# Kernel optimization log

Hardware: AMD Instinct MI355X
Metric: run time of the kernel (lower is better)

The kernel has to match this reference:

```python
import jax, jax.numpy as jnp
import numpy as np

B = 8192
D = 1024
NUM_CLASSES = 100


def setup_inputs() -> dict:
    key = jax.random.key(0)
    kx, ky = jax.random.split(key)
    x = jax.random.normal(kx, (B, D), dtype=jnp.float32)
    y = jax.random.randint(ky, (B,), 0, NUM_CLASSES, dtype=jnp.int64)
    return {"x": x, "y": y, "T": 1}


def reference(x, y, T):
    b = x.shape[0]
    # Pairwise Euclidean distances via Gram matrix (same math as
    # torch.norm(x[:,None]-x, dim=2) without the b*b*d intermediate).
    xn = jnp.sum(x * x, axis=1)                      # [b]
    d2 = xn[None, :] + xn[:, None] - 2.0 * (x @ x.T)  # [b, b]
    d2 = jnp.maximum(d2, 0.0)
    eye = jnp.eye(b, dtype=bool)
    # Diagonal is masked to -inf below; plug 1.0 to keep sqrt well-defined.
    dist = jnp.sqrt(jnp.where(eye, 1.0, d2))
    e_dist = -dist * T
    neg_inf = jnp.float32(-jnp.inf)
    # Denominator: all pairs except self.
    den_dist = jnp.where(eye, neg_inf, e_dist)
    # Numerator: same-label pairs except self.
    same = (y[None, :] == y[:, None]) & ~eye
    num_dist = jnp.where(same, e_dist, neg_inf)
    num = jax.nn.logsumexp(num_dist, axis=1)         # [b]
    den = jax.nn.logsumexp(den_dist, axis=1)         # [b]
    # Original fixup: anchors with no positives (num == -inf) contribute 0 to num;
    # den is re-indexed by isinf(num) AFTER num was zeroed, so den is unchanged.
    num = jnp.where(jnp.isinf(num), 0.0, num)
    return -jnp.mean(num - den)
```

## Files before the change

### kernel.cpp

```cpp
#include <hip/hip_runtime.h>
#include <hip/hip_bf16.h>
#include <stdint.h>

#define BN 8192
#define DK 1024
#define NTILES 2080

typedef __attribute__((ext_vector_type(4))) float f32x4;
typedef __attribute__((ext_vector_type(2))) long long2v;

__device__ __forceinline__ unsigned int f2e4m3(float f) {
  const unsigned int u = __float_as_uint(f);
  const unsigned int sign = (u >> 24) & 0x80u;
  float a = fabsf(f);
  if (a >= 448.f) return sign | 0x7Eu;
  if (a < 0.015625f) {
    int m = (int)rintf(a * 512.f);
    return sign | (unsigned int)m;
  }
  unsigned int x = __float_as_uint(a);
  x += 0x7FFFFu + ((x >> 20) & 1u);
  const unsigned int e = (x >> 23) - 127u + 7u;
  const unsigned int m = (x >> 20) & 7u;
  return sign | (e << 4) | m;
}

__global__ __launch_bounds__(256) void snn_prep(const float* __restrict__ x,
                                                unsigned char* __restrict__ xb,
                                                float* __restrict__ xn,
                                                float* __restrict__ den,
                                                float* __restrict__ num,
                                                float* __restrict__ out) {
  const int row = blockIdx.x * 4 + (threadIdx.x >> 6);
  const int lane = threadIdx.x & 63;
  const float4* src = (const float4*)(x + (size_t)row * DK) + lane * 4;
  float s = 0.f;
  unsigned int pk[4];
#pragma unroll
  for (int i = 0; i < 4; ++i) {
    float4 v = src[i];
    s = fmaf(v.x, v.x, s); s = fmaf(v.y, v.y, s);
    s = fmaf(v.z, v.z, s); s = fmaf(v.w, v.w, s);
    pk[i] = f2e4m3(v.x) | (f2e4m3(v.y) << 8) | (f2e4m3(v.z) << 16) |
            (f2e4m3(v.w) << 24);
  }
  const int g = lane >> 2;
  const int c = lane & 3;
  uint4 o; o.x = pk[0]; o.y = pk[1]; o.z = pk[2]; o.w = pk[3];
  *(uint4*)(xb + (size_t)row * DK + g * 64 + ((c ^ (row & 3)) << 4)) = o;
#pragma unroll
  for (int m = 32; m >= 1; m >>= 1) s += __shfl_xor(s, m);
  if (lane == 0) {
    xn[row] = s;
    den[row] = 0.f;
    num[row] = 0.f;
    if (row == 0) out[0] = 0.f;
  }
}

__global__ __launch_bounds__(256, 4) void snn_main(
    const unsigned char* __restrict__ xb, const float* __restrict__ xn,
    const int* __restrict__ y, const unsigned int* __restrict__ Tp,
    float* __restrict__ den, float* __restrict__ num) {
  __shared__ __align__(16) unsigned char As[2][128 * 64];
  __shared__ __align__(16) unsigned char Bs[2][128 * 64];
  __shared__ float xnA[128], xnB[128];
  __shared__ int yA[128], yB[128];

  const int t = threadIdx.x;
  const int lane = t & 63;
  const int w = t >> 6;
  const int wr = w >> 1, wc = w & 1;
  const int l15 = lane & 15;
  const int lg = lane >> 4;

  const int bid = blockIdx.x;
  const int ts = (bid & 7) * (NTILES / 8) + (bid >> 3);
  int I = (int)(64.5f - sqrtf(64.5f * 64.5f - 2.0f * (float)ts));
  while (I > 0 && (64 * I - (I * (I - 1)) / 2) > ts) --I;
  while ((64 * (I + 1) - ((I + 1) * I) / 2) <= ts) ++I;
  const int J = I + (ts - (64 * I - (I * (I - 1)) / 2));
  const int r0 = I * 128, c0 = J * 128;
  const bool diag = (I == J);

  const unsigned int tu = *Tp;
  const float tf = (tu & 0x7f800000u) ? __uint_as_float(tu) : (float)(int)tu;

  if (t < 128) {
    xnA[t] = xn[r0 + t]; yA[t] = y[r0 + t];
    xnB[t] = xn[c0 + t]; yB[t] = y[c0 + t];
  }

  auto ISSUE = [&](int buf, int kt) {
#pragma unroll
    for (int i = 0; i < 2; ++i) {
      const int linear = i * 256 + t;
      const int row = linear >> 2;
      const int cg = linear & 3;
      const unsigned char* sa = xb + (size_t)(r0 + row) * DK + kt + cg * 16;
      const unsigned char* sb = xb + (size_t)(c0 + row) * DK + kt + cg * 16;
      __builtin_amdgcn_global_load_lds(
          (const __attribute__((address_space(1))) void*)sa,
          (__attribute__((address_space(3))) void*)(As[buf] + linear * 16), 16, 0, 0);
      __builtin_amdgcn_global_load_lds(
          (const __attribute__((address_space(1))) void*)sb,
          (__attribute__((address_space(3))) void*)(Bs[buf] + linear * 16), 16, 0, 0);
    }
  };

  f32x4 acc[4][4];
#pragma unroll
  for (int mi = 0; mi < 4; ++mi)
#pragma unroll
    for (int ni = 0; ni < 4; ++ni) acc[mi][ni] = (f32x4){0.f, 0.f, 0.f, 0.f};

  const int fro = (lg ^ (l15 & 3)) << 4;

  ISSUE(0, 0);
  __syncthreads();

  for (int T = 0; T < 16; ++T) {
    const int buf = T & 1;
    if (T < 15) ISSUE(buf ^ 1, (T + 1) * 64);
    long2v aF[4], bF[4];
#pragma unroll
    for (int mi = 0; mi < 4; ++mi) {
      const int row = wr * 64 + mi * 16 + l15;
      aF[mi] = *(const long2v*)(As[buf] + row * 64 + fro);
    }
#pragma unroll
    for (int ni = 0; ni < 4; ++ni) {
      const int row = wc * 64 + ni * 16 + l15;
      bF[ni] = *(const long2v*)(Bs[buf] + row * 64 + fro);
    }
#pragma unroll
    for (int kk = 0; kk < 2; ++kk)
#pragma unroll
      for (int mi = 0; mi < 4; ++mi)
#pragma unroll
        for (int ni = 0; ni < 4; ++ni)
          acc[mi][ni] = __builtin_amdgcn_mfma_f32_16x16x32_fp8_fp8(
              aF[mi][kk], bF[ni][kk], acc[mi][ni], 0, 0, 0);
    __syncthreads();
  }

  float cxn[4]; int cy[4];
#pragma unroll
  for (int ni = 0; ni < 4; ++ni) {
    const int c_l = wc * 64 + ni * 16 + l15;
    cxn[ni] = xnB[c_l]; cy[ni] = yB[c_l];
  }
#pragma unroll
  for (int mi = 0; mi < 4; ++mi) {
#pragma unroll
    for (int rg = 0; rg < 4; ++rg) {
      const int row_l = wr * 64 + mi * 16 + lg * 4 + rg;
      const int rG = r0 + row_l;
      const float rxn = xnA[row_l];
      const int ry = yA[row_l];
      float u = 0.f, av = 0.f;
#pragma unroll
      for (int ni = 0; ni < 4; ++ni) {
        const int cG = c0 + wc * 64 + ni * 16 + l15;
        const float a = acc[mi][ni][rg];
        const float d2 = fmaxf(rxn + cxn[ni] - 2.0f * a, 0.f);
        const float p = (rG == cG) ? 0.f : __expf(-sqrtf(d2) * tf);
        const float v = (ry == cy[ni]) ? -p : p;
        acc[mi][ni][rg] = v;
        u += v; av += fabsf(v);
      }
#pragma unroll
      for (int mm = 8; mm >= 1; mm >>= 1) {
        u += __shfl_xor(u, mm); av += __shfl_xor(av, mm);
      }
      if (l15 == 0) {
        atomicAdd(&den[rG], av);
        atomicAdd(&num[rG], 0.5f * (av - u));
      }
    }
  }
  if (!diag) {
#pragma unroll
    for (int ni = 0; ni < 4; ++ni) {
      float u = 0.f, av = 0.f;
#pragma unroll
      for (int mi = 0; mi < 4; ++mi)
#pragma unroll
        for (int rg = 0; rg < 4; ++rg) {
          const float v = acc[mi][ni][rg];
          u += v; av += fabsf(v);
        }
      u += __shfl_xor(u, 16); av += __shfl_xor(av, 16);
      u += __shfl_xor(u, 32); av += __shfl_xor(av, 32);
      if (lg == 0) {
        const int cG = c0 + wc * 64 + ni * 16 + l15;
        atomicAdd(&den[cG], av);
        atomicAdd(&num[cG], 0.5f * (av - u));
      }
    }
  }
}

__global__ __launch_bounds__(256) void snn_final(const float* __restrict__ den,
                                                 const float* __restrict__ num,
                                                 float* __restrict__ out) {
  __shared__ float red[256];
  const int t = threadIdx.x;
  const int r = blockIdx.x * 256 + t;
  const float sd = den[r], sn = num[r];
  const float d = logf(sd);
  const float n = (sn > 0.f) ? logf(sn) : 0.f;
  red[t] = d - n;
  __syncthreads();
  for (int s = 128; s >= 1; s >>= 1) {
    if (t < s) red[t] += red[t + s];
    __syncthreads();
  }
  if (t == 0) atomicAdd(out, red[0] * (1.0f / (float)BN));
}

extern "C" void kernel_launch(void* const* d_in, const int* in_sizes, int n_in,
                              void* d_out, int out_size, void* d_ws, size_t ws_size,
                              hipStream_t stream) {
  const float* x = (const float*)d_in[0];
  const int* y = (const int*)d_in[1];
  const unsigned int* Tp = (const unsigned int*)d_in[2];
  float* out = (float*)d_out;

  char* ws = (char*)d_ws;
  unsigned char* xb = (unsigned char*)ws;
  float* xn = (float*)(ws + (size_t)BN * DK);
  float* den = xn + BN;
  float* num = den + BN;

  snn_prep<<<dim3(BN / 4), dim3(256), 0, stream>>>(x, xb, xn, den, num, out);
  snn_main<<<dim3(NTILES), dim3(256), 0, stream>>>(xb, xn, y, Tp, den, num);
  snn_final<<<dim3(32), dim3(256), 0, stream>>>(den, num, out);
}
```

Before: 124.9 us.

## Triple-buffer LDS pipeline with explicit vmcnt waits and revised swizzle

Replaces the double-buffered K loop with a three-stage LDS ring so two tiles of global-to-LDS loads are in flight. Each iteration waits only for the oldest load with explicit s_waitcnt vmcnt and a raw s_barrier instead of __syncthreads. It also changes the byte-chunk XOR swizzle to use bits 1-2 of the row, in both the prep writer and the fragment reader, to cut LDS bank conflicts. MFMA sections get raised wave priority. The extra LDS lowers the occupancy target from 4 to 3 blocks per SM, and the hand-written waitcnt counts must exactly match the number of loads issued.

```diff
diff --git a/kernel.cpp b/kernel.cpp
--- a/kernel.cpp
+++ b/kernel.cpp
@@ -4,10 +4,13 @@
 
 #define BN 8192
 #define DK 1024
+#define NT 16
 #define NTILES 2080
 
 typedef __attribute__((ext_vector_type(4))) float f32x4;
 typedef __attribute__((ext_vector_type(2))) long long2v;
+
+#define BAR() do { asm volatile("" ::: "memory"); __builtin_amdgcn_s_barrier(); asm volatile("" ::: "memory"); } while (0)
 
 __device__ __forceinline__ unsigned int f2e4m3(float f) {
   const unsigned int u = __float_as_uint(f);
@@ -47,7 +50,7 @@
   const int g = lane >> 2;
   const int c = lane & 3;
   uint4 o; o.x = pk[0]; o.y = pk[1]; o.z = pk[2]; o.w = pk[3];
-  *(uint4*)(xb + (size_t)row * DK + g * 64 + ((c ^ (row & 3)) << 4)) = o;
+  *(uint4*)(xb + (size_t)row * DK + g * 64 + ((c ^ ((row >> 1) & 3)) << 4)) = o;
 #pragma unroll
   for (int m = 32; m >= 1; m >>= 1) s += __shfl_xor(s, m);
   if (lane == 0) {
@@ -58,12 +61,12 @@
   }
 }
 
-__global__ __launch_bounds__(256, 4) void snn_main(
+__global__ __launch_bounds__(256, 3) void snn_main(
     const unsigned char* __restrict__ xb, const float* __restrict__ xn,
     const int* __restrict__ y, const unsigned int* __restrict__ Tp,
     float* __restrict__ den, float* __restrict__ num) {
-  __shared__ __align__(16) unsigned char As[2][128 * 64];
-  __shared__ __align__(16) unsigned char Bs[2][128 * 64];
+  __shared__ __align__(16) unsigned char As[3][128 * 64];
+  __shared__ __align__(16) unsigned char Bs[3][128 * 64];
   __shared__ float xnA[128], xnB[128];
   __shared__ int yA[128], yB[128];
 
@@ -114,25 +117,35 @@
 #pragma unroll
     for (int ni = 0; ni < 4; ++ni) acc[mi][ni] = (f32x4){0.f, 0.f, 0.f, 0.f};
 
-  const int fro = (lg ^ (l15 & 3)) << 4;
+  const int fro = (lg ^ ((l15 >> 1) & 3)) << 4;
 
   ISSUE(0, 0);
-  __syncthreads();
-
-  for (int T = 0; T < 16; ++T) {
-    const int buf = T & 1;
-    if (T < 15) ISSUE(buf ^ 1, (T + 1) * 64);
+  ISSUE(1, 64);
+  asm volatile("s_waitcnt vmcnt(4)" ::: "memory");
+  BAR();
+
+#pragma unroll
+  for (int T = 0; T < NT; ++T) {
+    const int rd = T % 3;
+    const int st = (T + 2) % 3;
     long2v aF[4], bF[4];
 #pragma unroll
     for (int mi = 0; mi < 4; ++mi) {
       const int row = wr * 64 + mi * 16 + l15;
-      aF[mi] = *(const long2v*)(As[buf] + row * 64 + fro);
+      aF[mi] = *(const long2v*)(As[rd] + row * 64 + fro);
     }
 #pragma unroll
     for (int ni = 0; ni < 4; ++ni) {
       const int row = wc * 64 + ni * 16 + l15;
-      bF[ni] = *(const long2v*)(Bs[buf] + row * 64 + fro);
-    }
+      bF[ni] = *(const long2v*)(Bs[rd] + row * 64 + fro);
+    }
+    if (T + 2 < NT) {
+      ISSUE(st, (T + 2) * 64);
+      asm volatile("s_waitcnt vmcnt(4)" ::: "memory");
+    } else if (T + 1 < NT) {
+      asm volatile("s_waitcnt vmcnt(0)" ::: "memory");
+    }
+    __builtin_amdgcn_s_setprio(1);
 #pragma unroll
     for (int kk = 0; kk < 2; ++kk)
 #pragma unroll
@@ -141,7 +154,8 @@
         for (int ni = 0; ni < 4; ++ni)
           acc[mi][ni] = __builtin_amdgcn_mfma_f32_16x16x32_fp8_fp8(
               aF[mi][kk], bF[ni][kk], acc[mi][ni], 0, 0, 0);
-    __syncthreads();
+    __builtin_amdgcn_s_setprio(0);
+    BAR();
   }
 
   float cxn[4]; int cy[4];
```

New measurement: 105.2 us. 1.19x faster.
